# Optimization experiments

Measured on AMD Instinct MI355X. Metric: run time of the kernel, lower is better.

## Reference

```python
import jax, jax.numpy as jnp
import numpy as np

B = 16384

def _linear_params(key, out_dim, in_dim):
    k1, k2 = jax.random.split(key)
    s = 1.0 / np.sqrt(in_dim)
    W = jax.random.uniform(k1, (out_dim, in_dim), jnp.float32, -s, s)
    b = jax.random.uniform(k2, (out_dim,), jnp.float32, -s, s)
    return W, b

def setup_inputs() -> dict:
    key = jax.random.key(0)
    ks = jax.random.split(key, 6)
    x = jax.random.normal(ks[0], (B, 784), jnp.float32)
    conv_w = jax.random.normal(ks[1], (3, 3), jnp.float32)
    W1, b1 = _linear_params(ks[2], 1024, 26 * 26)
    W2, b2 = _linear_params(ks[3], 512, 1024)
    W3, b3 = _linear_params(ks[4], 256, 512)
    W4, b4 = _linear_params(ks[5], 10, 256)
    return {"x": x, "conv_w": conv_w, "W1": W1, "b1": b1, "W2": W2, "b2": b2,
            "W3": W3, "b3": b3, "W4": W4, "b4": b4}

def reference(x, conv_w, W1, b1, W2, b2, W3, b3, W4, b4):
    b = x.shape[0]
    img = x.reshape(b, 1, 28, 28)                       # NCHW
    kern = conv_w.reshape(1, 1, 3, 3)                   # OIHW; cross-correlation
    y = jax.lax.conv_general_dilated(img, kern, (1, 1), 'VALID')  # [B,1,26,26]
    h = y.reshape(b, 26 * 26)
    h = jax.nn.relu(h @ W1.T + b1)
    h = jax.nn.relu(h @ W2.T + b2)
    h = jax.nn.relu(h @ W3.T + b3)
    return h @ W4.T + b4                                # [B,10] logits
```

## Files before the change

kernel.cpp:

```cpp
#include <hip/hip_runtime.h>
#include <hip/hip_bf16.h>
#include <stdint.h>

#define BDIM 256

typedef __attribute__((ext_vector_type(8))) short short8;
typedef __attribute__((ext_vector_type(4))) float f32x4;

#define AS1 __attribute__((address_space(1)))
#define AS3 __attribute__((address_space(3)))
#define GLL16(g, s) __builtin_amdgcn_global_load_lds((AS1 const void*)(g), (AS3 void*)(s), 16, 0, 0)

__device__ __forceinline__ unsigned short f2bf(float f) {
  union { float f; unsigned u; } v; v.f = f;
  unsigned r = v.u + 0x7fffu + ((v.u >> 16) & 1u);
  return (unsigned short)(r >> 16);
}
__device__ __forceinline__ float bf2f(unsigned short u) {
  union { unsigned u; float f; } v; v.u = ((unsigned)u) << 16;
  return v.f;
}

__global__ __launch_bounds__(BDIM) void cast_pad_w1(const float* __restrict__ w,
                                                    unsigned short* __restrict__ o) {
  int idx = blockIdx.x * BDIM + threadIdx.x;
  if (idx >= 1024 * 704) return;
  int n = idx / 704, k = idx - n * 704;
  float v = (k < 676) ? w[n * 676 + k] : 0.f;
  o[idx] = f2bf(v);
}

__global__ __launch_bounds__(BDIM) void cast_plain(const float* __restrict__ w,
                                                   unsigned short* __restrict__ o, int count) {
  int idx = blockIdx.x * BDIM + threadIdx.x;
  if (idx < count) o[idx] = f2bf(w[idx]);
}

__global__ __launch_bounds__(BDIM) void conv3x3(const float* __restrict__ x,
                                                const float* __restrict__ cw,
                                                unsigned short* __restrict__ h0) {
  __shared__ float xs[784];
  __shared__ float w[9];
  int m = blockIdx.x;
  const float* xr = x + (size_t)m * 784;
  if (threadIdx.x < 9) w[threadIdx.x] = cw[threadIdx.x];
  for (int i = threadIdx.x; i < 784; i += BDIM) xs[i] = xr[i];
  __syncthreads();
  unsigned short* hr = h0 + (size_t)m * 704;
  for (int p = threadIdx.x; p < 704; p += BDIM) {
    float v = 0.f;
    if (p < 676) {
      int r = p / 26, c = p - r * 26;
      const float* xp = &xs[r * 28 + c];
      v = xp[0]  * w[0] + xp[1]  * w[1] + xp[2]  * w[2]
        + xp[28] * w[3] + xp[29] * w[4] + xp[30] * w[5]
        + xp[56] * w[6] + xp[57] * w[7] + xp[58] * w[8];
    }
    hr[p] = f2bf(v);
  }
}

template <bool RELU>
__global__ __launch_bounds__(BDIM) void gemm_bt(const unsigned short* __restrict__ A,
                                                const unsigned short* __restrict__ Wt,
                                                const float* __restrict__ bias,
                                                unsigned short* __restrict__ Cb,
                                                int M, int N, int K) {
  __shared__ unsigned short As[2][128 * 32];
  __shared__ unsigned short Bs[2][128 * 32];
  const int tid = threadIdx.x;
  const int lane = tid & 63;
  const int wid = tid >> 6;
  const int nbm = M >> 7;
  const int brow = (blockIdx.x % nbm) << 7;
  const int bcol = (blockIdx.x / nbm) << 7;

  const int srow = (wid << 4) + (lane >> 2);
  const int scol = (lane & 3) << 3;
  const unsigned short* gA0 = A + (size_t)(brow + srow) * K + scol;
  const unsigned short* gA1 = A + (size_t)(brow + 64 + srow) * K + scol;
  const unsigned short* gB0 = Wt + (size_t)(bcol + srow) * K + scol;
  const unsigned short* gB1 = Wt + (size_t)(bcol + 64 + srow) * K + scol;
  const int ldsoff = wid << 9;

#define STAGE(buf, koff)                                   \
  do {                                                     \
    GLL16(gA0 + (koff), &As[buf][ldsoff]);                 \
    GLL16(gA1 + (koff), &As[buf][2048 + ldsoff]);          \
    GLL16(gB0 + (koff), &Bs[buf][ldsoff]);                 \
    GLL16(gB1 + (koff), &Bs[buf][2048 + ldsoff]);          \
  } while (0)

  f32x4 acc[4][4] = {};

  const int wr = (wid >> 1) << 6;
  const int wc = (wid & 1) << 6;
  const int fr = lane & 15;
  const int fk = (lane >> 4) << 3;
  const int aoff = (wr + fr) * 32 + fk;
  const int boff = (wc + fr) * 32 + fk;

  const int nk = K >> 5;
  STAGE(0, 0);
  __syncthreads();
  int cur = 0;
  for (int kt = 0; kt < nk; ++kt) {
    if (kt + 1 < nk) STAGE(cur ^ 1, (kt + 1) * 32);
    const unsigned short* pa = &As[cur][aoff];
    const unsigned short* pb = &Bs[cur][boff];
    short8 af[4], bf[4];
#pragma unroll
    for (int m = 0; m < 4; ++m) af[m] = *(const short8*)(pa + m * 512);
#pragma unroll
    for (int n = 0; n < 4; ++n) bf[n] = *(const short8*)(pb + n * 512);
#pragma unroll
    for (int m = 0; m < 4; ++m)
#pragma unroll
      for (int n = 0; n < 4; ++n)
        acc[m][n] = __builtin_amdgcn_mfma_f32_16x16x32_bf16(af[m], bf[n], acc[m][n], 0, 0, 0);
    __syncthreads();
    cur ^= 1;
  }
#undef STAGE

  const int crow = brow + wr + ((lane >> 4) << 2);
  const int ccol0 = bcol + wc + (lane & 15);
#pragma unroll
  for (int n = 0; n < 4; ++n) {
    const int cc = ccol0 + n * 16;
    const float bv = bias[cc];
#pragma unroll
    for (int m = 0; m < 4; ++m) {
      const int rr = crow + m * 16;
#pragma unroll
      for (int j = 0; j < 4; ++j) {
        float v = acc[m][n][j] + bv;
        if (RELU) v = v > 0.f ? v : 0.f;
        Cb[(size_t)(rr + j) * N + cc] = f2bf(v);
      }
    }
  }
}

__global__ __launch_bounds__(BDIM) void fc10(const unsigned short* __restrict__ h3,
                                             const float* __restrict__ W4,
                                             const float* __restrict__ b4,
                                             float* __restrict__ out) {
  int lane = threadIdx.x & 63;
  int wid = threadIdx.x >> 6;
  int m = blockIdx.x * 4 + wid;
  const unsigned short* hr = h3 + (size_t)m * 256 + lane * 4;
  uint64_t hv = *(const uint64_t*)hr;
  float e0 = bf2f((unsigned short)hv), e1 = bf2f((unsigned short)(hv >> 16));
  float e2 = bf2f((unsigned short)(hv >> 32)), e3 = bf2f((unsigned short)(hv >> 48));
#pragma unroll
  for (int n = 0; n < 10; ++n) {
    const float4 wv = *(const float4*)(W4 + n * 256 + lane * 4);
    float s = e0 * wv.x + e1 * wv.y + e2 * wv.z + e3 * wv.w;
#pragma unroll
    for (int off = 32; off > 0; off >>= 1) s += __shfl_xor(s, off);
    if (lane == n) out[(size_t)m * 10 + n] = s + b4[n];
  }
}

extern "C" void kernel_launch(void* const* d_in, const int* in_sizes, int n_in,
                              void* d_out, int out_size, void* d_ws, size_t ws_size,
                              hipStream_t stream) {
  const float* x  = (const float*)d_in[0];
  const float* cw = (const float*)d_in[1];
  const float* W1 = (const float*)d_in[2];
  const float* b1 = (const float*)d_in[3];
  const float* W2 = (const float*)d_in[4];
  const float* b2 = (const float*)d_in[5];
  const float* W3 = (const float*)d_in[6];
  const float* b3 = (const float*)d_in[7];
  const float* W4 = (const float*)d_in[8];
  const float* b4 = (const float*)d_in[9];
  float* out = (float*)d_out;

  char* ws = (char*)d_ws;
  unsigned short* h0  = (unsigned short*)(ws);
  unsigned short* h1  = (unsigned short*)(ws + 23068672);
  unsigned short* W1b = (unsigned short*)(ws + 23068672 + 33554432);
  unsigned short* W2b = W1b + 1024 * 704;
  unsigned short* W3b = W2b + 512 * 1024;
  unsigned short* h2  = h0;
  unsigned short* h3  = h1;

  cast_pad_w1<<<2816, BDIM, 0, stream>>>(W1, W1b);
  cast_plain<<<2048, BDIM, 0, stream>>>(W2, W2b, 512 * 1024);
  cast_plain<<<512, BDIM, 0, stream>>>(W3, W3b, 256 * 512);
  conv3x3<<<16384, BDIM, 0, stream>>>(x, cw, h0);

  gemm_bt<true><<<(16384 / 128) * (1024 / 128), BDIM, 0, stream>>>(h0, W1b, b1, h1, 16384, 1024, 704);
  gemm_bt<true><<<(16384 / 128) * (512 / 128),  BDIM, 0, stream>>>(h1, W2b, b2, h2, 16384, 512, 1024);
  gemm_bt<true><<<(16384 / 128) * (256 / 128),  BDIM, 0, stream>>>(h2, W3b, b3, h3, 16384, 256, 512);
  fc10<<<16384 / 4, BDIM, 0, stream>>>(h3, W4, b4, out);
}
```

Baseline: 131.9 us.

## Use larger templated GEMM tiles with 512 threads and K-step 64

Swaps the fixed 128x128x32 GEMM with 256 threads for a templated kernel running 8 waves. Its per-layer tile shapes are 256x256, 256x128 and 128x128, and each stage covers 64 K elements. Bigger tiles raise data reuse per LDS load and halve the number of barriers per K. In exchange it uses much more LDS (up to 128KB double-buffered for 256x256) and more accumulator registers, which may cut occupancy. The unpadded LDS layout with a 64-element row stride may also cause bank conflicts.

```diff
diff --git a/kernel.cpp b/kernel.cpp
--- a/kernel.cpp
+++ b/kernel.cpp
@@ -60,78 +60,84 @@
   }
 }
 
-template <bool RELU>
-__global__ __launch_bounds__(BDIM) void gemm_bt(const unsigned short* __restrict__ A,
-                                                const unsigned short* __restrict__ Wt,
-                                                const float* __restrict__ bias,
-                                                unsigned short* __restrict__ Cb,
-                                                int M, int N, int K) {
-  __shared__ unsigned short As[2][128 * 32];
-  __shared__ unsigned short Bs[2][128 * 32];
+template <int BM, int BN, int WGM, bool RELU>
+__global__ __launch_bounds__(512, 2) void gemm_bt2(const unsigned short* __restrict__ A,
+                                                   const unsigned short* __restrict__ Wt,
+                                                   const float* __restrict__ bias,
+                                                   unsigned short* __restrict__ Cb,
+                                                   int M, int N, int K) {
+  constexpr int WGN = 8 / WGM;
+  constexpr int FM = BM / WGM / 16;
+  constexpr int FN = BN / WGN / 16;
+  constexpr int RA = BM / 64;
+  constexpr int RB = BN / 64;
+  __shared__ unsigned short As[2][BM * 64];
+  __shared__ unsigned short Bs[2][BN * 64];
   const int tid = threadIdx.x;
   const int lane = tid & 63;
   const int wid = tid >> 6;
-  const int nbm = M >> 7;
-  const int brow = (blockIdx.x % nbm) << 7;
-  const int bcol = (blockIdx.x / nbm) << 7;
-
-  const int srow = (wid << 4) + (lane >> 2);
-  const int scol = (lane & 3) << 3;
-  const unsigned short* gA0 = A + (size_t)(brow + srow) * K + scol;
-  const unsigned short* gA1 = A + (size_t)(brow + 64 + srow) * K + scol;
-  const unsigned short* gB0 = Wt + (size_t)(bcol + srow) * K + scol;
-  const unsigned short* gB1 = Wt + (size_t)(bcol + 64 + srow) * K + scol;
-  const int ldsoff = wid << 9;
-
-#define STAGE(buf, koff)                                   \
-  do {                                                     \
-    GLL16(gA0 + (koff), &As[buf][ldsoff]);                 \
-    GLL16(gA1 + (koff), &As[buf][2048 + ldsoff]);          \
-    GLL16(gB0 + (koff), &Bs[buf][ldsoff]);                 \
-    GLL16(gB1 + (koff), &Bs[buf][2048 + ldsoff]);          \
+  const int nbm = M / BM;
+  const int brow = (blockIdx.x % nbm) * BM;
+  const int bcol = (blockIdx.x / nbm) * BN;
+
+  const int srow = tid >> 3;
+  const int scol = (tid & 7) << 3;
+  const unsigned short* gA = A + (size_t)(brow + srow) * K + scol;
+  const unsigned short* gB = Wt + (size_t)(bcol + srow) * K + scol;
+  const int sdst = tid * 8;
+
+#define STAGE(buf, kt)                                                        \
+  do {                                                                        \
+    _Pragma("unroll")                                                         \
+    for (int r = 0; r < RA; ++r)                                              \
+      GLL16(gA + (size_t)r * 64 * K + (kt) * 64, &As[buf][r * 4096 + sdst]);  \
+    _Pragma("unroll")                                                         \
+    for (int r = 0; r < RB; ++r)                                              \
+      GLL16(gB + (size_t)r * 64 * K + (kt) * 64, &Bs[buf][r * 4096 + sdst]);  \
   } while (0)
 
-  f32x4 acc[4][4] = {};
-
-  const int wr = (wid >> 1) << 6;
-  const int wc = (wid & 1) << 6;
+  f32x4 acc[FM][FN] = {};
+
   const int fr = lane & 15;
-  const int fk = (lane >> 4) << 3;
-  const int aoff = (wr + fr) * 32 + fk;
-  const int boff = (wc + fr) * 32 + fk;
-
-  const int nk = K >> 5;
+  const int g8 = (lane >> 4) << 3;
+  const int abase = (wid / WGN) * (FM * 16);
+  const int bbase = (wid % WGN) * (FN * 16);
+
+  const int nk = K >> 6;
   STAGE(0, 0);
   __syncthreads();
   int cur = 0;
   for (int kt = 0; kt < nk; ++kt) {
-    if (kt + 1 < nk) STAGE(cur ^ 1, (kt + 1) * 32);
-    const unsigned short* pa = &As[cur][aoff];
-    const unsigned short* pb = &Bs[cur][boff];
-    short8 af[4], bf[4];
-#pragma unroll
-    for (int m = 0; m < 4; ++m) af[m] = *(const short8*)(pa + m * 512);
-#pragma unroll
-    for (int n = 0; n < 4; ++n) bf[n] = *(const short8*)(pb + n * 512);
-#pragma unroll
-    for (int m = 0; m < 4; ++m)
-#pragma unroll
-      for (int n = 0; n < 4; ++n)
-        acc[m][n] = __builtin_amdgcn_mfma_f32_16x16x32_bf16(af[m], bf[n], acc[m][n], 0, 0, 0);
+    if (kt + 1 < nk) STAGE(cur ^ 1, kt + 1);
+#pragma unroll
+    for (int s = 0; s < 2; ++s) {
+      short8 af[FM], bf[FN];
+#pragma unroll
+      for (int m = 0; m < FM; ++m)
+        af[m] = *(const short8*)&As[cur][(abase + m * 16 + fr) * 64 + s * 32 + g8];
+#pragma unroll
+      for (int n = 0; n < FN; ++n)
+        bf[n] = *(const short8*)&Bs[cur][(bbase + n * 16 + fr) * 64 + s * 32 + g8];
+#pragma unroll
+      for (int m = 0; m < FM; ++m)
+#pragma unroll
+        for (int n = 0; n < FN; ++n)
+          acc[m][n] = __builtin_amdgcn_mfma_f32_16x16x32_bf16(af[m], bf[n], acc[m][n], 0, 0, 0);
+    }
     __syncthreads();
     cur ^= 1;
   }
 #undef STAGE
 
-  const int crow = brow + wr + ((lane >> 4) << 2);
-  const int ccol0 = bcol + wc + (lane & 15);
-#pragma unroll
-  for (int n = 0; n < 4; ++n) {
+  const int crow0 = brow + abase + ((lane >> 4) << 2);
+  const int ccol0 = bcol + bbase + fr;
+#pragma unroll
+  for (int n = 0; n < FN; ++n) {
     const int cc = ccol0 + n * 16;
     const float bv = bias[cc];
 #pragma unroll
-    for (int m = 0; m < 4; ++m) {
-      const int rr = crow + m * 16;
+    for (int m = 0; m < FM; ++m) {
+      const int rr = crow0 + m * 16;
 #pragma unroll
       for (int j = 0; j < 4; ++j) {
         float v = acc[m][n][j] + bv;
@@ -192,8 +198,11 @@
   cast_plain<<<512, BDIM, 0, stream>>>(W3, W3b, 256 * 512);
   conv3x3<<<16384, BDIM, 0, stream>>>(x, cw, h0);
 
-  gemm_bt<true><<<(16384 / 128) * (1024 / 128), BDIM, 0, stream>>>(h0, W1b, b1, h1, 16384, 1024, 704);
-  gemm_bt<true><<<(16384 / 128) * (512 / 128),  BDIM, 0, stream>>>(h1, W2b, b2, h2, 16384, 512, 1024);
-  gemm_bt<true><<<(16384 / 128) * (256 / 128),  BDIM, 0, stream>>>(h2, W3b, b3, h3, 16384, 256, 512);
+  gemm_bt2<256, 256, 2, true><<<(16384 / 256) * (1024 / 256), 512, 0, stream>>>(
+      h0, W1b, b1, h1, 16384, 1024, 704);
+  gemm_bt2<256, 128, 4, true><<<(16384 / 256) * (512 / 128), 512, 0, stream>>>(
+      h1, W2b, b2, h2, 16384, 512, 1024);
+  gemm_bt2<128, 128, 4, true><<<(16384 / 128) * (256 / 128), 512, 0, stream>>>(
+      h2, W3b, b3, h3, 16384, 256, 512);
   fc10<<<16384 / 4, BDIM, 0, stream>>>(h3, W4, b4, out);
 }
```

Measured after the change: 135.3 us. +2.6%, slower.
